# Kernel optimization log

Measured on AMD Instinct MI355X. Metric: run time of the kernel, lower is better.

Reference implementation:

```python
import jax
import jax.numpy as jnp
from jax import lax
import numpy as np

B, C, Wd, Hd = 32, 2048, 7, 7


def setup_inputs() -> dict:
    key = jax.random.key(0)
    k1, k2, k3 = jax.random.split(key, 3)
    x = jax.random.normal(k1, (B, C, Wd, Hd), dtype=jnp.float32)
    # Conv2d(C, C, 3, 1, 1): kaiming-like scale for stability
    conv_w = jax.random.normal(k2, (C, C, 3, 3), dtype=jnp.float32) * (1.0 / np.sqrt(C * 9))
    conv_b = jax.random.normal(k3, (C,), dtype=jnp.float32) * 0.01
    return {"x": x, "conv_w": conv_w, "conv_b": conv_b}


def reference(x, conv_w, conv_b):
    b, c, w, h = x.shape
    n = w * h
    xf = x.reshape(b, c, n)  # [B, C, WH]
    # bilinear channel similarity: [B, C, C]
    bilinear = jnp.einsum('bcn,bdn->bcd', xf, xf) / n
    # softmax over negated similarity along last dim
    W_SCI = jax.nn.softmax(-bilinear, axis=2)
    # attention-weighted channel mix: [B, C, WH]
    Y = jnp.einsum('bcd,bdn->bcn', W_SCI, xf)
    # 3x3 conv, stride 1, padding 1 (SAME)
    Yc = lax.conv_general_dilated(
        Y.reshape(b, c, w, h), conv_w,
        window_strides=(1, 1), padding='SAME',
        dimension_numbers=('NCHW', 'OIHW', 'NCHW'))
    Yc = Yc + conv_b[None, :, None, None]
    Z = Yc.reshape(b, c, n) + xf  # residual
    return Z
```

## Files before the change

kernel.cpp:

```cpp
#include <hip/hip_runtime.h>
#include <stdint.h>

#define BB 32
#define CC 2048
#define NPIX 49
#define KPAD 64

typedef __bf16 bf16;
typedef __bf16 bf16x4 __attribute__((ext_vector_type(4)));
typedef __bf16 bf16x8 __attribute__((ext_vector_type(8)));
typedef float f32x4 __attribute__((ext_vector_type(4)));
typedef uint32_t u32x4 __attribute__((ext_vector_type(4)));
typedef long i64;

#define MFMA(a,b,c) __builtin_amdgcn_mfma_f32_16x16x32_bf16(a,b,c,0,0,0)
#define MFMA8(a,b,c) __builtin_amdgcn_mfma_f32_16x16x32_fp8_fp8(a,b,c,0,0,0)
#define GLOAD_LDS(g, l) __builtin_amdgcn_global_load_lds( \
    (const __attribute__((address_space(1))) void*)(g),   \
    (__attribute__((address_space(3))) void*)(l), 16, 0, 0)

__global__ void prep_fused_kernel(const float* __restrict__ x,
                                  bf16* __restrict__ xb, bf16* __restrict__ xbT) {
    __shared__ float xt[6272];
    const int tid = threadIdx.x;
    const int b = blockIdx.x >> 4, cb = blockIdx.x & 15;
    const float* src = x + ((size_t)(b * 2048 + cb * 128)) * 49;
#pragma unroll
    for (int i = 0; i < 25; i++) {
        int idx = i * 256 + tid;
        if (idx < 6272) xt[idx] = src[idx];
    }
    __syncthreads();
    {
        const int r = tid >> 1, h = tid & 1;
        bf16* dst = xb + ((size_t)(b * 2048 + cb * 128 + r)) * 64 + h * 32;
        const float* row = &xt[r * 49];
#pragma unroll
        for (int v = 0; v < 4; v++) {
            bf16x8 o;
#pragma unroll
            for (int e = 0; e < 8; e++) {
                int n = h * 32 + v * 8 + e;
                o[e] = (bf16)(n < 49 ? row[n] : 0.f);
            }
            *(bf16x8*)(dst + v * 8) = o;
        }
    }
    {
        const int n = tid >> 2, q = tid & 3;
        bf16* dst = xbT + ((size_t)b * 64 + n) * 2048 + cb * 128 + q * 32;
#pragma unroll
        for (int v = 0; v < 4; v++) {
            bf16x8 o;
#pragma unroll
            for (int e = 0; e < 8; e++) {
                int cl = q * 32 + v * 8 + e;
                o[e] = (bf16)(n < 49 ? xt[cl * 49 + n] : 0.f);
            }
            *(bf16x8*)(dst + v * 8) = o;
        }
    }
}

__global__ void castw_wino_kernel(const float* __restrict__ cw, uint8_t* __restrict__ Uw) {
    uint32_t t = blockIdx.x * 256u + threadIdx.x;
    uint32_t q = t & 511u, co = t >> 9;
    uint32_t ci0 = q * 4u;
    const f32x4* src4 = (const f32x4*)(cw + ((size_t)co * 2048u + ci0) * 9u);
    float g[36];
#pragma unroll
    for (int m = 0; m < 9; m++) {
        f32x4 t4 = src4[m];
#pragma unroll
        for (int e = 0; e < 4; e++) g[m * 4 + e] = t4[e];
    }
    float u[16][4];
#pragma unroll
    for (int c4 = 0; c4 < 4; c4++) {
        const float* gg = g + c4 * 9;
        float tr[4][3];
#pragma unroll
        for (int col = 0; col < 3; col++) {
            float a0 = gg[col], a1 = gg[3 + col], a2 = gg[6 + col];
            tr[0][col] = a0;
            tr[1][col] = 0.5f * (a0 + a1 + a2);
            tr[2][col] = 0.5f * (a0 - a1 + a2);
            tr[3][col] = a2;
        }
#pragma unroll
        for (int r = 0; r < 4; r++) {
            u[r * 4 + 0][c4] = tr[r][0];
            u[r * 4 + 1][c4] = 0.5f * (tr[r][0] + tr[r][1] + tr[r][2]);
            u[r * 4 + 2][c4] = 0.5f * (tr[r][0] - tr[r][1] + tr[r][2]);
            u[r * 4 + 3][c4] = tr[r][2];
        }
    }
#pragma unroll
    for (int e = 0; e < 16; e++) {
        int p = __builtin_amdgcn_cvt_pk_fp8_f32(u[e][0] * 16.f, u[e][1] * 16.f, 0, false);
        p = __builtin_amdgcn_cvt_pk_fp8_f32(u[e][2] * 16.f, u[e][3] * 16.f, p, true);
        *(uint32_t*)(Uw + (size_t)e * 4194304u + (size_t)co * 2048u + ci0) = (uint32_t)p;
    }
}

__global__ __launch_bounds__(512, 2) void attn_kernel(
    const bf16* __restrict__ xb, const bf16* __restrict__ xbT, bf16* __restrict__ YpT)
{
    __shared__ __align__(16) char smem[67584];
    bf16* Ktile = (bf16*)smem;
    bf16* Vtile = (bf16*)(smem + 16384);
    bf16 (*Plds)[16][136] = reinterpret_cast<bf16(*)[16][136]>(smem + 32768);
    bf16 (*Tlds)[132] = reinterpret_cast<bf16(*)[132]>(smem);

    const int tid = threadIdx.x;
    const int w = tid >> 6, l = tid & 63;
    const int lhi = l >> 4, llo = l & 15;
    const uint32_t g = blockIdx.x;
    const int xcd = g & 7, inner = g >> 3;
    const int b = xcd + (inner >> 4) * 8;
    const int cblk = inner & 15;
    const int c0 = cblk * 128 + w * 16;
    const bf16* xbB = xb + (size_t)b * CC * KPAD;
    const bf16* xbTB = xbT + (size_t)b * KPAD * CC;

    {
        int h = tid >> 4, c16 = tid & 15;
        int row;
        if (h < 9) row = h;
        else if (h < 18) row = 63 + h;
        else { int p = h - 18; row = 9 * ((p >> 1) + 1) + (p & 1) * 8; }
        u32x4 z4 = {0, 0, 0, 0};
        *(u32x4*)(YpT + ((size_t)b * 81 + row) * CC + cblk * 128 + c16 * 8) = z4;
    }

    bf16x8 aQ[2];
#pragma unroll
    for (int kk = 0; kk < 2; kk++)
        aQ[kk] = *(const bf16x8*)(xbB + (uint32_t)(c0 + llo) * KPAD + kk * 32 + lhi * 8);

    const uint32_t rowK = tid >> 3;
    const uint32_t srcKoff = (uint32_t)(((tid & 7u) ^ (rowK & 7u)) << 3);
    const bf16* kSrc = xbB + (size_t)rowK * KPAD + srcKoff;
    const uint32_t rowV = tid >> 4;
    const uint32_t srcVoff = (uint32_t)(((tid & 15u) ^ (rowV & 7u)) << 3);
    const bf16* vSrc = xbTB + (size_t)rowV * CC + srcVoff;

    f32x4 accY[4];
#pragma unroll
    for (int nf = 0; nf < 4; nf++) accY[nf] = (f32x4){0, 0, 0, 0};
    float rowsum[4] = {};

    const float kES = -0.029442756956917622f;

    for (int dt = 0; dt < 16; dt++) {
        const int d0 = dt * 128;
#pragma unroll
        for (int i = 0; i < 2; i++) {
            GLOAD_LDS(kSrc + (size_t)(d0 + i * 64) * KPAD, (char*)Ktile + i * 8192 + tid * 16);
            GLOAD_LDS(vSrc + d0 + (size_t)i * 32 * CC,     (char*)Vtile + i * 8192 + tid * 16);
        }
        __syncthreads();

        f32x4 accS[8];
#pragma unroll
        for (int df = 0; df < 8; df++) accS[df] = (f32x4){0, 0, 0, 0};
#pragma unroll
        for (int kk = 0; kk < 2; kk++) {
#pragma unroll
            for (int df = 0; df < 8; df++) {
                uint32_t r = (uint32_t)(df * 16 + llo);
                bf16x8 bK = *(const bf16x8*)((const char*)Ktile + r * 128u +
                                             ((((uint32_t)(kk * 4 + lhi)) ^ (r & 7u)) << 4));
                accS[df] = MFMA(aQ[kk], bK, accS[df]);
            }
        }
#pragma unroll
        for (int df = 0; df < 8; df++)
#pragma unroll
            for (int r = 0; r < 4; r++) {
                float p = __builtin_amdgcn_exp2f(accS[df][r] * kES);
                rowsum[r] += p;
                Plds[w][lhi * 4 + r][df * 16 + llo] = (bf16)p;
            }
#pragma unroll
        for (int kk2 = 0; kk2 < 4; kk2++) {
            bf16x8 aP = *(const bf16x8*)&Plds[w][llo][kk2 * 32 + lhi * 8];
#pragma unroll
            for (int nf = 0; nf < 4; nf++) {
                uint32_t r = (uint32_t)(nf * 16 + llo);
                bf16x8 bV = *(const bf16x8*)((const char*)Vtile + r * 256u +
                                             ((((uint32_t)(kk2 * 4 + lhi)) ^ (r & 7u)) << 4));
                accY[nf] = MFMA(aP, bV, accY[nf]);
            }
        }
        __syncthreads();
    }
#pragma unroll
    for (int r = 0; r < 4; r++) {
        float s = rowsum[r];
        s += __shfl_xor(s, 1);
        s += __shfl_xor(s, 2);
        s += __shfl_xor(s, 4);
        s += __shfl_xor(s, 8);
        rowsum[r] = 1.0f / s;
    }
    __syncthreads();
#pragma unroll
    for (int nf = 0; nf < 4; nf++)
#pragma unroll
        for (int r = 0; r < 4; r++) {
            int n = nf * 16 + llo;
            int cl = w * 16 + lhi * 4 + r;
            Tlds[n][cl] = (bf16)(accY[nf][r] * rowsum[r]);
        }
    __syncthreads();
#pragma unroll
    for (int rr = 0; rr < 7; rr++) {
        int row = rr * 8 + w;
        if (row < NPIX) {
            int i = row / 7, j = row % 7;
            int sp = (i + 1) * 9 + (j + 1);
            int col2 = tid & 63;
            uint32_t val = *(const uint32_t*)&Tlds[row][col2 * 2];
            *(uint32_t*)(YpT + ((size_t)b * 81 + sp) * CC + cblk * 128 + col2 * 2) = val;
        }
    }
}

__global__ void wino_in_kernel(const bf16* __restrict__ YpT, uint8_t* __restrict__ Ux) {
    const int n = blockIdx.x;
    const int b = n >> 4, t = n & 15, ti = t >> 2, tj = t & 3;
    const int c0 = threadIdx.x * 4;
    float d[4][4][4];
#pragma unroll
    for (int di = 0; di < 4; di++) {
        int spi = 2 * ti + di; if (spi > 8) spi = 8;
#pragma unroll
        for (int dj = 0; dj < 4; dj++) {
            int spj = 2 * tj + dj; if (spj > 8) spj = 8;
            bf16x4 v = *(const bf16x4*)(YpT + ((size_t)b * 81 + spi * 9 + spj) * 2048 + c0);
#pragma unroll
            for (int k = 0; k < 4; k++) d[di][dj][k] = (float)v[k];
        }
    }
    float R[4][4][4];
#pragma unroll
    for (int dj = 0; dj < 4; dj++)
#pragma unroll
        for (int k = 0; k < 4; k++) {
            R[0][dj][k] = d[0][dj][k] - d[2][dj][k];
            R[1][dj][k] = d[1][dj][k] + d[2][dj][k];
            R[2][dj][k] = d[2][dj][k] - d[1][dj][k];
            R[3][dj][k] = d[1][dj][k] - d[3][dj][k];
        }
#pragma unroll
    for (int r = 0; r < 4; r++) {
#pragma unroll
        for (int k = 0; k < 4; k++) {
            float v0 = R[r][0][k] - R[r][2][k];
            float v1 = R[r][1][k] + R[r][2][k];
            float v2 = R[r][2][k] - R[r][1][k];
            float v3 = R[r][1][k] - R[r][3][k];
            R[r][0][k] = v0; R[r][1][k] = v1; R[r][2][k] = v2; R[r][3][k] = v3;
        }
#pragma unroll
        for (int cc = 0; cc < 4; cc++) {
            int p = __builtin_amdgcn_cvt_pk_fp8_f32(R[r][cc][0] * 4.f, R[r][cc][1] * 4.f, 0, false);
            p = __builtin_amdgcn_cvt_pk_fp8_f32(R[r][cc][2] * 4.f, R[r][cc][3] * 4.f, p, true);
            *(uint32_t*)(Ux + (size_t)(r * 4 + cc) * 1048576u + (size_t)n * 2048 + c0) = (uint32_t)p;
        }
    }
}

#define CONV_BARRIER() do { __builtin_amdgcn_sched_barrier(0); \
    __builtin_amdgcn_s_barrier(); __builtin_amdgcn_sched_barrier(0); } while (0)
#define CONV_VMW(n) asm volatile("s_waitcnt vmcnt(" #n ")" ::: "memory")

#define WSTAGE(bufOff, t, kh) do {                                             \
    uint32_t kA_ = (uint32_t)(t) * 128u + (uint32_t)(kh) * 64u;                \
    _Pragma("unroll")                                                          \
    for (int i_ = 0; i_ < 2; i_++) {                                           \
        GLOAD_LDS(srcA[i_] + kA_,                                              \
                  smem + (bufOff) + (kh) * 16384 + i_ * 8192 + tid * 16);      \
        GLOAD_LDS(srcB[i_] + kA_,                                              \
                  smem + (bufOff) + 32768 + (kh) * 16384 + i_ * 8192 + tid * 16); \
    }                                                                          \
} while (0)

#define CONV_PHASE(bufOff, kk, GATE, STAGE_STMT) do {                          \
    CONV_VMW(GATE);                                                            \
    CONV_BARRIER();                                                            \
    i64 af[8][2], bfr[4][2];                                                   \
    _Pragma("unroll")                                                          \
    for (int f = 0; f < 8; f++)                                                \
        _Pragma("unroll")                                                      \
        for (int s = 0; s < 2; s++)                                            \
            af[f][s] = *(const i64*)(smem + (bufOff) + (kk) * 16384 + offA[f][s]); \
    _Pragma("unroll")                                                          \
    for (int f = 0; f < 4; f++)                                                \
        _Pragma("unroll")                                                      \
        for (int s = 0; s < 2; s++)                                            \
            bfr[f][s] = *(const i64*)(smem + (bufOff) + 32768 + (kk) * 16384 + offB[f][s]); \
    STAGE_STMT;                                                                \
    asm volatile("s_waitcnt lgkmcnt(0)" ::: "memory");                         \
    __builtin_amdgcn_sched_barrier(0);                                         \
    __builtin_amdgcn_s_setprio(1);                                             \
    _Pragma("unroll")                                                          \
    for (int s = 0; s < 2; s++)                                                \
        _Pragma("unroll")                                                      \
        for (int fm = 0; fm < 8; fm++)                                         \
            _Pragma("unroll")                                                  \
            for (int fn = 0; fn < 4; fn++)                                     \
                acc[fm][fn] = MFMA8(af[fm][s], bfr[fn][s], acc[fm][fn]);       \
    __builtin_amdgcn_s_setprio(0);                                             \
    __builtin_amdgcn_sched_barrier(0);                                         \
} while (0)

__global__ __launch_bounds__(512, 2) void wino_gemm_kernel(
    const uint8_t* __restrict__ Ux, const uint8_t* __restrict__ Uw, bf16* __restrict__ Vt)
{
    extern __shared__ __align__(16) char smem[];
    const int tid = threadIdx.x;
    const int w = tid >> 6, l = tid & 63;
    const int lhi = l >> 4, llo = l & 15;
    const int wm = w >> 2, wn = w & 3;

    uint32_t g = blockIdx.x;
    uint32_t xcd = g & 7u, inner = g >> 3;
    uint32_t e = xcd * 2u + (inner >> 4);
    uint32_t sub = inner & 15u;
    uint32_t mt = sub >> 3, nt = sub & 7u;

    uint32_t rowLoc = tid >> 2;
    uint32_t slot = tid & 3u;
    const uint8_t* srcA[2];
    const uint8_t* srcB[2];
#pragma unroll
    for (int i = 0; i < 2; i++) {
        uint32_t row = (uint32_t)i * 128u + rowLoc;
        uint32_t swz = (uint32_t)((slot ^ ((row >> 1) & 3u)) << 4);
        srcA[i] = Ux + (size_t)e * 1048576u + (size_t)(mt * 256u + row) * 2048u + swz;
        srcB[i] = Uw + (size_t)e * 4194304u + (size_t)(nt * 256u + row) * 2048u + swz;
    }

    uint32_t offA[8][2], offB[4][2];
#pragma unroll
    for (int f = 0; f < 8; f++) {
        uint32_t r = (uint32_t)(wm * 128 + f * 16 + llo);
#pragma unroll
        for (int s = 0; s < 2; s++) {
            uint32_t q = ((uint32_t)(2 * s + (lhi >> 1))) ^ ((r >> 1) & 3u);
            offA[f][s] = r * 64u + (q << 4) + ((uint32_t)(lhi & 1) << 3);
        }
    }
#pragma unroll
    for (int f = 0; f < 4; f++) {
        uint32_t r = (uint32_t)(wn * 64 + f * 16 + llo);
#pragma unroll
        for (int s = 0; s < 2; s++) {
            uint32_t q = ((uint32_t)(2 * s + (lhi >> 1))) ^ ((r >> 1) & 3u);
            offB[f][s] = r * 64u + (q << 4) + ((uint32_t)(lhi & 1) << 3);
        }
    }

    f32x4 acc[8][4];
#pragma unroll
    for (int fm = 0; fm < 8; fm++)
#pragma unroll
        for (int fn = 0; fn < 4; fn++) acc[fm][fn] = (f32x4){0, 0, 0, 0};

    WSTAGE(0, 0, 0);
    WSTAGE(0, 0, 1);
    WSTAGE(65536, 1, 0);

    for (int it = 0; it < 7; ++it) {
        const int t0 = it * 2;
        CONV_PHASE(0,     0, 8, WSTAGE(65536, t0 + 1, 1));
        CONV_PHASE(0,     1, 8, WSTAGE(0,     t0 + 2, 0));
        CONV_PHASE(65536, 0, 8, WSTAGE(0,     t0 + 2, 1));
        CONV_PHASE(65536, 1, 8, WSTAGE(65536, t0 + 3, 0));
    }
    CONV_PHASE(0,     0, 8, WSTAGE(65536, 15, 1));
    CONV_PHASE(0,     1, 8, (void)0);
    CONV_PHASE(65536, 0, 4, (void)0);
    CONV_PHASE(65536, 1, 0, (void)0);

    bf16* pz = Vt + (size_t)e * 1048576u;
    uint32_t n0 = mt * 256u + (uint32_t)(wm * 128 + lhi * 4);
    uint32_t co0 = nt * 256u + (uint32_t)(wn * 64 + llo);
#pragma unroll
    for (int fm = 0; fm < 8; fm++)
#pragma unroll
        for (int fn = 0; fn < 4; fn++)
#pragma unroll
            for (int r = 0; r < 4; r++)
                pz[(size_t)(n0 + fm * 16u + r) * 2048u + (co0 + fn * 16u)] =
                    (bf16)acc[fm][fn][r];
}

__global__ void wino_out_kernel(const bf16* __restrict__ Vt, const float* __restrict__ x,
                                const float* __restrict__ cb, float* __restrict__ out)
{
    __shared__ float Ml[16][16][33];
    __shared__ float Ol[32][50];
    __shared__ float cbl[32];
    const int tid = threadIdx.x;
    const int b = blockIdx.x >> 6, cg = blockIdx.x & 63;
    const int c0 = cg * 32;

    {
        int e = tid >> 4, t = tid & 15;
        const bf16* src = Vt + ((size_t)e * 512 + b * 16 + t) * 2048 + c0;
#pragma unroll
        for (int v = 0; v < 4; v++) {
            bf16x8 vv = *(const bf16x8*)(src + v * 8);
#pragma unroll
            for (int k = 0; k < 8; k++) Ml[e][t][v * 8 + k] = (float)vv[k] * 0.015625f;
        }
    }
    if (tid < 32) cbl[tid] = cb[c0 + tid];
    __syncthreads();

    {
        int t = tid & 15, cp = tid >> 4;
        int ti = t >> 2, tj = t & 3;
#pragma unroll
        for (int cc2 = 0; cc2 < 2; cc2++) {
            int cc = cp * 2 + cc2;
            float M[16];
#pragma unroll
            for (int e = 0; e < 16; e++) M[e] = Ml[e][t][cc];
            float s0[4], s1[4];
#pragma unroll
            for (int col = 0; col < 4; col++) {
                s0[col] = M[col] + M[4 + col] + M[8 + col];
                s1[col] = M[4 + col] - M[8 + col] - M[12 + col];
            }
            float y00 = s0[0] + s0[1] + s0[2];
            float y01 = s0[1] - s0[2] - s0[3];
            float y10 = s1[0] + s1[1] + s1[2];
            float y11 = s1[1] - s1[2] - s1[3];
            int i0 = 2 * ti, j0 = 2 * tj;
            Ol[cc][i0 * 7 + j0] = y00;
            if (j0 + 1 < 7) Ol[cc][i0 * 7 + j0 + 1] = y01;
            if (i0 + 1 < 7) Ol[cc][(i0 + 1) * 7 + j0] = y10;
            if (i0 + 1 < 7 && j0 + 1 < 7) Ol[cc][(i0 + 1) * 7 + j0 + 1] = y11;
        }
    }
    __syncthreads();

    {
        const float* xs = x + ((size_t)b * 2048 + c0) * 49;
        float* os = out + ((size_t)b * 2048 + c0) * 49;
        for (int k = tid; k < 1568; k += 256) {
            int c = k / 49, p = k - c * 49;
            os[k] = Ol[c][p] + cbl[c] + xs[k];
        }
    }
}

extern "C" void kernel_launch(void* const* d_in, const int* in_sizes, int n_in,
                              void* d_out, int out_size, void* d_ws, size_t ws_size,
                              hipStream_t stream) {
    (void)in_sizes; (void)n_in; (void)out_size; (void)ws_size;
    const float* x = (const float*)d_in[0];
    const float* cw = (const float*)d_in[1];
    const float* cb = (const float*)d_in[2];
    float* out = (float*)d_out;
    char* ws = (char*)d_ws;

    bf16* xb     = (bf16*)(ws);
    bf16* xbT    = (bf16*)(ws + 8388608);
    uint8_t* Ux  = (uint8_t*)(ws);
    bf16* YpT    = (bf16*)(ws + 16777216);
    uint8_t* Uw  = (uint8_t*)(ws + 27525120);
    bf16* Vt     = (bf16*)(ws + 94633984);

    hipFuncSetAttribute((const void*)wino_gemm_kernel,
                        hipFuncAttributeMaxDynamicSharedMemorySize, 131072);

    prep_fused_kernel<<<512, 256, 0, stream>>>(x, xb, xbT);
    castw_wino_kernel<<<4096, 256, 0, stream>>>(cw, Uw);
    attn_kernel<<<512, 512, 0, stream>>>(xb, xbT, YpT);
    wino_in_kernel<<<512, 512, 0, stream>>>(YpT, Ux);
    wino_gemm_kernel<<<256, 512, 131072, stream>>>(Ux, Uw, Vt);
    wino_out_kernel<<<2048, 256, 0, stream>>>(Vt, x, cb, out);
}
```

Measured before the change: 229.5 us.

## Fuse Winograd input transform into attention epilogue and widen GEMM LDS reads

```diff
diff --git a/kernel.cpp b/kernel.cpp
--- a/kernel.cpp
+++ b/kernel.cpp
@@ -12,12 +12,18 @@
 typedef float f32x4 __attribute__((ext_vector_type(4)));
 typedef uint32_t u32x4 __attribute__((ext_vector_type(4)));
 typedef long i64;
+typedef long i64x2 __attribute__((ext_vector_type(2)));
 
 #define MFMA(a,b,c) __builtin_amdgcn_mfma_f32_16x16x32_bf16(a,b,c,0,0,0)
 #define MFMA8(a,b,c) __builtin_amdgcn_mfma_f32_16x16x32_fp8_fp8(a,b,c,0,0,0)
 #define GLOAD_LDS(g, l) __builtin_amdgcn_global_load_lds( \
     (const __attribute__((address_space(1))) void*)(g),   \
     (__attribute__((address_space(3))) void*)(l), 16, 0, 0)
+
+__device__ __forceinline__ uint32_t kperm(uint32_t c) {
+    uint32_t local = c & 63u, s = local >> 5, lh = (local >> 3) & 3u, o8 = local & 7u;
+    return (c & ~63u) | (lh * 16u + s * 8u + o8);
+}
 
 __global__ void prep_fused_kernel(const float* __restrict__ x,
                                   bf16* __restrict__ xb, bf16* __restrict__ xbT) {
@@ -66,6 +72,7 @@
     uint32_t t = blockIdx.x * 256u + threadIdx.x;
     uint32_t q = t & 511u, co = t >> 9;
     uint32_t ci0 = q * 4u;
+    uint32_t nci = kperm(ci0);
     const f32x4* src4 = (const f32x4*)(cw + ((size_t)co * 2048u + ci0) * 9u);
     float g[36];
 #pragma unroll
@@ -99,12 +106,12 @@
     for (int e = 0; e < 16; e++) {
         int p = __builtin_amdgcn_cvt_pk_fp8_f32(u[e][0] * 16.f, u[e][1] * 16.f, 0, false);
         p = __builtin_amdgcn_cvt_pk_fp8_f32(u[e][2] * 16.f, u[e][3] * 16.f, p, true);
-        *(uint32_t*)(Uw + (size_t)e * 4194304u + (size_t)co * 2048u + ci0) = (uint32_t)p;
+        *(uint32_t*)(Uw + (size_t)e * 4194304u + (size_t)co * 2048u + nci) = (uint32_t)p;
     }
 }
 
 __global__ __launch_bounds__(512, 2) void attn_kernel(
-    const bf16* __restrict__ xb, const bf16* __restrict__ xbT, bf16* __restrict__ YpT)
+    const bf16* __restrict__ xb, const bf16* __restrict__ xbT, uint8_t* __restrict__ Ux)
 {
     __shared__ __align__(16) char smem[67584];
     bf16* Ktile = (bf16*)smem;
@@ -123,16 +130,6 @@
     const bf16* xbB = xb + (size_t)b * CC * KPAD;
     const bf16* xbTB = xbT + (size_t)b * KPAD * CC;
 
-    {
-        int h = tid >> 4, c16 = tid & 15;
-        int row;
-        if (h < 9) row = h;
-        else if (h < 18) row = 63 + h;
-        else { int p = h - 18; row = 9 * ((p >> 1) + 1) + (p & 1) * 8; }
-        u32x4 z4 = {0, 0, 0, 0};
-        *(u32x4*)(YpT + ((size_t)b * 81 + row) * CC + cblk * 128 + c16 * 8) = z4;
-    }
-
     bf16x8 aQ[2];
 #pragma unroll
     for (int kk = 0; kk < 2; kk++)
@@ -214,60 +211,57 @@
             Tlds[n][cl] = (bf16)(accY[nf][r] * rowsum[r]);
         }
     __syncthreads();
-#pragma unroll
-    for (int rr = 0; rr < 7; rr++) {
-        int row = rr * 8 + w;
-        if (row < NPIX) {
-            int i = row / 7, j = row % 7;
-            int sp = (i + 1) * 9 + (j + 1);
-            int col2 = tid & 63;
-            uint32_t val = *(const uint32_t*)&Tlds[row][col2 * 2];
-            *(uint32_t*)(YpT + ((size_t)b * 81 + sp) * CC + cblk * 128 + col2 * 2) = val;
-        }
-    }
-}
-
-__global__ void wino_in_kernel(const bf16* __restrict__ YpT, uint8_t* __restrict__ Ux) {
-    const int n = blockIdx.x;
-    const int b = n >> 4, t = n & 15, ti = t >> 2, tj = t & 3;
-    const int c0 = threadIdx.x * 4;
-    float d[4][4][4];
-#pragma unroll
-    for (int di = 0; di < 4; di++) {
-        int spi = 2 * ti + di; if (spi > 8) spi = 8;
-#pragma unroll
-        for (int dj = 0; dj < 4; dj++) {
-            int spj = 2 * tj + dj; if (spj > 8) spj = 8;
-            bf16x4 v = *(const bf16x4*)(YpT + ((size_t)b * 81 + spi * 9 + spj) * 2048 + c0);
-#pragma unroll
-            for (int k = 0; k < 4; k++) d[di][dj][k] = (float)v[k];
-        }
-    }
-    float R[4][4][4];
-#pragma unroll
-    for (int dj = 0; dj < 4; dj++)
-#pragma unroll
-        for (int k = 0; k < 4; k++) {
-            R[0][dj][k] = d[0][dj][k] - d[2][dj][k];
-            R[1][dj][k] = d[1][dj][k] + d[2][dj][k];
-            R[2][dj][k] = d[2][dj][k] - d[1][dj][k];
-            R[3][dj][k] = d[1][dj][k] - d[3][dj][k];
-        }
-#pragma unroll
-    for (int r = 0; r < 4; r++) {
-#pragma unroll
-        for (int k = 0; k < 4; k++) {
-            float v0 = R[r][0][k] - R[r][2][k];
-            float v1 = R[r][1][k] + R[r][2][k];
-            float v2 = R[r][2][k] - R[r][1][k];
-            float v3 = R[r][1][k] - R[r][3][k];
-            R[r][0][k] = v0; R[r][1][k] = v1; R[r][2][k] = v2; R[r][3][k] = v3;
-        }
-#pragma unroll
-        for (int cc = 0; cc < 4; cc++) {
-            int p = __builtin_amdgcn_cvt_pk_fp8_f32(R[r][cc][0] * 4.f, R[r][cc][1] * 4.f, 0, false);
-            p = __builtin_amdgcn_cvt_pk_fp8_f32(R[r][cc][2] * 4.f, R[r][cc][3] * 4.f, p, true);
-            *(uint32_t*)(Ux + (size_t)(r * 4 + cc) * 1048576u + (size_t)n * 2048 + c0) = (uint32_t)p;
+
+    {
+        const int t = tid >> 5;
+        const int clg = tid & 31;
+        const int cl0 = clg * 4;
+        const int ti = t >> 2, tj = t & 3;
+        float d[4][4][4];
+#pragma unroll
+        for (int di = 0; di < 4; di++) {
+            int i = 2 * ti + di - 1;
+#pragma unroll
+            for (int dj = 0; dj < 4; dj++) {
+                int j = 2 * tj + dj - 1;
+                if (i >= 0 && i < 7 && j >= 0 && j < 7) {
+                    bf16x4 v = *(const bf16x4*)&Tlds[i * 7 + j][cl0];
+#pragma unroll
+                    for (int k = 0; k < 4; k++) d[di][dj][k] = (float)v[k];
+                } else {
+#pragma unroll
+                    for (int k = 0; k < 4; k++) d[di][dj][k] = 0.f;
+                }
+            }
+        }
+        float R[4][4][4];
+#pragma unroll
+        for (int dj = 0; dj < 4; dj++)
+#pragma unroll
+            for (int k = 0; k < 4; k++) {
+                R[0][dj][k] = d[0][dj][k] - d[2][dj][k];
+                R[1][dj][k] = d[1][dj][k] + d[2][dj][k];
+                R[2][dj][k] = d[2][dj][k] - d[1][dj][k];
+                R[3][dj][k] = d[1][dj][k] - d[3][dj][k];
+            }
+        uint32_t nci = kperm((uint32_t)(cblk * 128 + cl0));
+        uint8_t* dst = Ux + (size_t)(b * 16 + t) * 2048 + nci;
+#pragma unroll
+        for (int r = 0; r < 4; r++) {
+            float V[4][4];
+#pragma unroll
+            for (int k = 0; k < 4; k++) {
+                V[0][k] = (R[r][0][k] - R[r][2][k]) * 4.f;
+                V[1][k] = (R[r][1][k] + R[r][2][k]) * 4.f;
+                V[2][k] = (R[r][2][k] - R[r][1][k]) * 4.f;
+                V[3][k] = (R[r][1][k] - R[r][3][k]) * 4.f;
+            }
+#pragma unroll
+            for (int cc = 0; cc < 4; cc++) {
+                int p = __builtin_amdgcn_cvt_pk_fp8_f32(V[cc][0], V[cc][1], 0, false);
+                p = __builtin_amdgcn_cvt_pk_fp8_f32(V[cc][2], V[cc][3], p, true);
+                *(uint32_t*)(dst + (size_t)(r * 4 + cc) * 1048576u) = (uint32_t)p;
+            }
         }
     }
 }
@@ -290,17 +284,13 @@
 #define CONV_PHASE(bufOff, kk, GATE, STAGE_STMT) do {                          \
     CONV_VMW(GATE);                                                            \
     CONV_BARRIER();                                                            \
-    i64 af[8][2], bfr[4][2];                                                   \
+    i64x2 af[8], bfr[4];                                                       \
     _Pragma("unroll")                                                          \
     for (int f = 0; f < 8; f++)                                                \
-        _Pragma("unroll")                                                      \
-        for (int s = 0; s < 2; s++)                                            \
-            af[f][s] = *(const i64*)(smem + (bufOff) + (kk) * 16384 + offA[f][s]); \
+        af[f] = *(const i64x2*)(smem + (bufOff) + (kk) * 16384 + offA[f]);     \
     _Pragma("unroll")                                                          \
     for (int f = 0; f < 4; f++)                                                \
-        _Pragma("unroll")                                                      \
-        for (int s = 0; s < 2; s++)                                            \
-            bfr[f][s] = *(const i64*)(smem + (bufOff) + 32768 + (kk) * 16384 + offB[f][s]); \
+        bfr[f] = *(const i64x2*)(smem + (bufOff) + 32768 + (kk) * 16384 + offB[f]); \
     STAGE_STMT;                                                                \
     asm volatile("s_waitcnt lgkmcnt(0)" ::: "memory");                         \
     __builtin_amdgcn_sched_barrier(0);                                         \
@@ -343,24 +333,16 @@
         srcB[i] = Uw + (size_t)e * 4194304u + (size_t)(nt * 256u + row) * 2048u + swz;
     }
 
-    uint32_t offA[8][2], offB[4][2];
+    uint32_t offA[8], offB[4];
 #pragma unroll
     for (int f = 0; f < 8; f++) {
         uint32_t r = (uint32_t)(wm * 128 + f * 16 + llo);
-#pragma unroll
-        for (int s = 0; s < 2; s++) {
-            uint32_t q = ((uint32_t)(2 * s + (lhi >> 1))) ^ ((r >> 1) & 3u);
-            offA[f][s] = r * 64u + (q << 4) + ((uint32_t)(lhi & 1) << 3);
-        }
+        offA[f] = r * 64u + (uint32_t)(((uint32_t)lhi ^ ((r >> 1) & 3u)) << 4);
     }
 #pragma unroll
     for (int f = 0; f < 4; f++) {
         uint32_t r = (uint32_t)(wn * 64 + f * 16 + llo);
-#pragma unroll
-        for (int s = 0; s < 2; s++) {
-            uint32_t q = ((uint32_t)(2 * s + (lhi >> 1))) ^ ((r >> 1) & 3u);
-            offB[f][s] = r * 64u + (q << 4) + ((uint32_t)(lhi & 1) << 3);
-        }
+        offB[f] = r * 64u + (uint32_t)(((uint32_t)lhi ^ ((r >> 1) & 3u)) << 4);
     }
 
     f32x4 acc[8][4];
@@ -471,18 +453,16 @@
 
     bf16* xb     = (bf16*)(ws);
     bf16* xbT    = (bf16*)(ws + 8388608);
-    uint8_t* Ux  = (uint8_t*)(ws);
-    bf16* YpT    = (bf16*)(ws + 16777216);
-    uint8_t* Uw  = (uint8_t*)(ws + 27525120);
-    bf16* Vt     = (bf16*)(ws + 94633984);
+    uint8_t* Ux  = (uint8_t*)(ws + 16777216);
+    uint8_t* Uw  = (uint8_t*)(ws + 33554432);
+    bf16* Vt     = (bf16*)(ws + 100663296);
 
     hipFuncSetAttribute((const void*)wino_gemm_kernel,
                         hipFuncAttributeMaxDynamicSharedMemorySize, 131072);
 
     prep_fused_kernel<<<512, 256, 0, stream>>>(x, xb, xbT);
     castw_wino_kernel<<<4096, 256, 0, stream>>>(cw, Uw);
-    attn_kernel<<<512, 512, 0, stream>>>(xb, xbT, YpT);
-    wino_in_kernel<<<512, 512, 0, stream>>>(YpT, Ux);
+    attn_kernel<<<512, 512, 0, stream>>>(xb, xbT, Ux);
     wino_gemm_kernel<<<256, 512, 131072, stream>>>(Ux, Uw, Vt);
     wino_out_kernel<<<2048, 256, 0, stream>>>(Vt, x, cb, out);
 }
```

Result: faster. 185.1 us, median of 3 (-19.4%).
